# Kernel tuning notes

Measured on AMD Instinct MI355X. Metric: run time of the kernel, lower is better.

## Reference

```python
import jax, jax.numpy as jnp
import numpy as np

EPS = 1e-6

def elu1(x):
    return jax.nn.elu(x) + 1.0

def causal_linear_attention(q, k, v, chunk=128):
    # q,k,v: [b,h,s,d]; standard (elu+1) linear attention with causal cumulative
    # normalization, computed chunk-wise with a lax.scan carrying the kv state.
    b, h, s, d = q.shape
    sq, sk = elu1(q), elu1(k)
    nc = s // chunk
    rs = lambda x: x.reshape(b, h, nc, chunk, d).transpose(2, 0, 1, 3, 4)  # [nc,b,h,L,d]
    sqc, skc, vc = rs(sq), rs(sk), rs(v)
    mask = jnp.tril(jnp.ones((chunk, chunk), dtype=q.dtype))

    def step(carry, xs):
        S, z = carry  # S: [b,h,d,d] running sum of k^T v; z: [b,h,d] running sum of k
        qc, kc, vcc = xs
        scores = jnp.einsum('bhid,bhjd->bhij', qc, kc) * mask
        num = jnp.einsum('bhij,bhje->bhie', scores, vcc) + jnp.einsum('bhid,bhde->bhie', qc, S)
        den = scores.sum(-1) + jnp.einsum('bhid,bhd->bhi', qc, z)
        out = num / jnp.clip(den, EPS)[..., None]
        S = S + jnp.einsum('bhjd,bhje->bhde', kc, vcc)
        z = z + kc.sum(2)
        return (S, z), out

    S0 = jnp.zeros((b, h, d, d), q.dtype)
    z0 = jnp.zeros((b, h, d), q.dtype)
    _, outs = jax.lax.scan(step, (S0, z0), (sqc, skc, vc))
    return outs.transpose(1, 2, 0, 3, 4).reshape(b, h, s, d)

def setup_inputs() -> dict:
    B, S, H, NH, NM = 2, 4096, 2048, 16, 4
    HD = H // NH
    key = jax.random.key(0)
    ks = jax.random.split(key, 12)
    p = lambda k, shp: (jax.random.normal(k, shp, dtype=jnp.float32) * 0.02)
    return {
        'hidden_states': jax.random.normal(ks[0], (B, S, H), dtype=jnp.float32),
        'w_q': p(ks[1], (H, H)),
        'w_k': p(ks[2], (H, H)),
        'w_v': p(ks[3], (H, H)),
        'w_o': p(ks[4], (H, H)),
        'eg_w1': p(ks[5], (H // 4, H)),
        'eg_b1': jnp.zeros((H // 4,), jnp.float32),
        'eg_w2': p(ks[6], (1, H // 4)),
        'eg_b2': jnp.zeros((1,), jnp.float32),
        'memory_gate': jnp.zeros((NH,), jnp.float32),
        'fine_memories': jax.random.uniform(ks[7], (NM, NH, HD, HD), dtype=jnp.float32) * 0.1,
        'fine_memory_norms': jax.random.uniform(ks[8], (NM, NH, HD), dtype=jnp.float32) + 0.1,
    }

def reference(hidden_states, w_q, w_k, w_v, w_o, eg_w1, eg_b1, eg_w2, eg_b2,
              memory_gate, fine_memories, fine_memory_norms):
    B, S, H = hidden_states.shape
    NH = memory_gate.shape[0]
    HD = H // NH
    split = lambda x: x.reshape(B, S, NH, HD).transpose(0, 2, 1, 3)  # [b,h,s,d]
    q = split(hidden_states @ w_q.T)
    k = split(hidden_states @ w_k.T)
    v = split(hidden_states @ w_v.T)
    sq = elu1(q)

    # coarse memory = sum of fine banks
    M = fine_memories.sum(0)            # [h,d,d]
    z = fine_memory_norms.sum(0)        # [h,d]
    a_c = jnp.einsum('bhsd,hde->bhse', sq, M)
    n_c = jnp.clip(jnp.einsum('bhsd,hd->bhs', sq, z), EPS)[..., None]
    out_coarse = jnp.where(z.sum() < EPS, 0.0, a_c / n_c)

    # fine-grained retrieval over banks, softmax-weighted by relevance
    a_f = jnp.einsum('bhsd,mhde->mbhse', sq, fine_memories)
    n_f = jnp.einsum('bhsd,mhd->mbhs', sq, fine_memory_norms)
    bank_dead = (fine_memory_norms.sum((1, 2)) < EPS)[:, None, None, None, None]
    outs = jnp.where(bank_dead, 0.0, a_f / jnp.clip(n_f, EPS)[..., None])
    rel = n_f.mean(-1)  # [m,b,h]
    w = jax.nn.softmax(rel, axis=0)[..., None, None]  # [m,b,h,1,1]
    out_fine = (outs * w).sum(0)

    # learned expansion gate from coarse representation
    coarse_repr = out_coarse.transpose(0, 2, 1, 3).reshape(B, S, H)
    gprob = jax.nn.sigmoid(jax.nn.relu(coarse_repr @ eg_w1.T + eg_b1) @ eg_w2.T + eg_b2)  # [b,s,1]
    exp_prob = gprob.transpose(0, 2, 1)[..., None]  # [b,1,s,1]

    memory_output = exp_prob * out_fine + (1.0 - exp_prob) * out_coarse
    local_output = causal_linear_attention(q, k, v)
    gate = jax.nn.sigmoid(memory_gate).reshape(1, NH, 1, 1)
    output = gate * memory_output + (1.0 - gate) * local_output
    output = output.transpose(0, 2, 1, 3).reshape(B, S, H)
    return output @ w_o.T
```

## Files before the change

kernel.cpp:

```cpp
#include <hip/hip_runtime.h>

typedef unsigned short ush;
typedef short s16x8 __attribute__((ext_vector_type(8)));
typedef float f32x4 __attribute__((ext_vector_type(4)));

#define Bv 2
#define Sv 4096
#define Hv 2048
#define NHv 16
#define HDv 128
#define NMv 4
#define Tv (Bv*Sv)
#define CHv 128
#define NCv (Sv/CHv)
#define EPSf 1e-6f
#define NTHc ((size_t)Tv*Hv)

__device__ __forceinline__ float b2f(ush u){ return __uint_as_float(((unsigned)u)<<16); }
__device__ __forceinline__ ush f2b(float f){
  unsigned x = __float_as_uint(f);
  return (ush)((x + 0x7fffu + ((x>>16)&1u)) >> 16);
}
__device__ __forceinline__ float lo16(unsigned u){ return b2f((ush)(u & 0xffffu)); }
__device__ __forceinline__ float hi16(unsigned u){ return b2f((ush)(u >> 16)); }
__device__ __forceinline__ unsigned pack2(float a, float b){ return (unsigned)f2b(a) | ((unsigned)f2b(b) << 16); }
__device__ __forceinline__ float elu1f(float x){ return x > 0.f ? x + 1.f : __expf(x); }
__device__ __forceinline__ float sigm(float x){ return 1.f/(1.f + __expf(-x)); }

__device__ __forceinline__ void gload_lds16(const ush* g, ush* l) {
  __builtin_amdgcn_global_load_lds((const __attribute__((address_space(1))) unsigned int*)g,
                                   (__attribute__((address_space(3))) unsigned int*)l, 16, 0, 0);
}

__global__ void probe_kernel(float* out, float val){ out[0] = val; }

__global__ __launch_bounds__(256)
void cvt_kernel(const float* __restrict__ in, ush* __restrict__ out, int n8)
{
  int i = blockIdx.x * 256 + threadIdx.x;
  if (i >= n8) return;
  const float4* p = (const float4*)in + (size_t)i*2;
  float4 x = p[0], y = p[1];
  ushort4 a; a.x=f2b(x.x); a.y=f2b(x.y); a.z=f2b(x.z); a.w=f2b(x.w);
  ushort4 b; b.x=f2b(y.x); b.y=f2b(y.y); b.z=f2b(y.z); b.w=f2b(y.w);
  *(ushort4*)(out + (size_t)i*8)     = a;
  *(ushort4*)(out + (size_t)i*8 + 4) = b;
}

__global__ __launch_bounds__(256)
void fmt_kernel(const float* __restrict__ fm, ush* __restrict__ fmt)
{
  int mh = blockIdx.x;
  const float* src = fm + (size_t)mh*HDv*HDv;
  ush* dst = fmt + (size_t)mh*HDv*HDv;
  __shared__ ush T[HDv][HDv+4];
  #pragma unroll 4
  for (int l = 0; l < 64; ++l) {
    int idx = threadIdx.x + l*256;
    int d = idx >> 7, e = idx & 127;
    T[d][e] = f2b(src[idx]);
  }
  __syncthreads();
  #pragma unroll 4
  for (int l = 0; l < 64; ++l) {
    int idx = threadIdx.x + l*256;
    int e = idx >> 7, d = idx & 127;
    dst[idx] = T[d][e];
  }
}

__global__ __launch_bounds__(256)
void tp_kernel(const ush* __restrict__ src, ush* __restrict__ dst)
{
  int blk = blockIdx.x;
  int st = blk & 31, bh = blk >> 5;
  int h = bh & 15, b = bh >> 4;
  size_t t0 = (size_t)b*Sv + st*128;
  int hcol = h*HDv;
  __shared__ __align__(16) ush T[128*128];
  int tid = threadIdx.x;
  #pragma unroll
  for (int l = 0; l < 8; ++l) {
    int idx = tid + l*256;
    int row = idx >> 4, c8 = (idx & 15) << 3;
    *(uint4*)(T + row*128 + c8) = *(const uint4*)(src + (t0 + row)*Hv + hcol + c8);
  }
  __syncthreads();
  #pragma unroll
  for (int l = 0; l < 8; ++l) {
    int idx = tid + l*256;
    int d = idx & 127, t8 = (idx >> 7) << 3;
    ush tmp[8];
    #pragma unroll
    for (int q = 0; q < 8; ++q) tmp[q] = T[(t8 + q)*128 + d];
    *(uint4*)(dst + ((size_t)bh*HDv + d)*Sv + st*128 + t8) = *(uint4*)tmp;
  }
}

template<int OBF, int EPQ>
__global__ __launch_bounds__(512)
void gemm8(const ush* __restrict__ A, const ush* __restrict__ B,
           const float* __restrict__ bias,
           ush* __restrict__ C0, ush* __restrict__ C1, ush* __restrict__ C2,
           float* __restrict__ Cf, int N, int K)
{
  __shared__ __align__(16) ush LDS[3*16384 + 3*8192];
  ush* Atb = LDS;
  ush* Btb = LDS + 3*16384;
  const int tid = threadIdx.x, lane = tid & 63, w = tid >> 6;
  const int wr = w >> 1, wn = w & 1;
  const int la = lane & 15, lk = lane >> 4;

  int bid = blockIdx.x;
  int NBX = N >> 7;
  int by, bx;
  if ((NBX & 7) == 0) {
    int bpx = NBX >> 3;
    int xcd = bid & 7;
    int idx = bid >> 3;
    bx = xcd*bpx + idx % bpx;
    by = idx / bpx;
  } else {
    bx = bid % NBX;
    by = bid / NBX;
  }
  int bm = by << 8, bn = bx << 7;

  auto stage = [&](int t){
    int kt = t << 6;
    ush* Ad = Atb + (t % 3) * 16384;
    ush* Bd = Btb + (t % 3) * 8192;
    #pragma unroll
    for (int c = 0; c < 4; ++c) {
      int idx = tid + c*512;
      int row = idx >> 3, sl = idx & 7;
      gload_lds16(A + (size_t)(bm + row)*K + kt + ((sl ^ (row & 7))*8),
                  Ad + (w*64 + c*512)*8);
    }
    #pragma unroll
    for (int c = 0; c < 2; ++c) {
      int idx = tid + c*512;
      int row = idx >> 3, sl = idx & 7;
      gload_lds16(B + (size_t)(bn + row)*K + kt + ((sl ^ (row & 7))*8),
                  Bd + (w*64 + c*512)*8);
    }
  };

  f32x4 acc[4][4];
  #pragma unroll
  for (int i = 0; i < 4; ++i)
    #pragma unroll
    for (int j = 0; j < 4; ++j) acc[i][j] = (f32x4){0.f,0.f,0.f,0.f};

  stage(0);
  stage(1);
  const int nt = 32;
  for (int t = 0; t < nt; ++t) {
    if (t < nt-2) {
      stage(t + 2);
      asm volatile("s_waitcnt vmcnt(12)" ::: "memory");
    } else if (t == nt-2) {
      asm volatile("s_waitcnt vmcnt(6)" ::: "memory");
    } else {
      asm volatile("s_waitcnt vmcnt(0)" ::: "memory");
    }
    __builtin_amdgcn_s_barrier();
    __builtin_amdgcn_sched_barrier(0);

    const ush* Ab = Atb + (t % 3) * 16384;
    const ush* Bb = Btb + (t % 3) * 8192;
    __builtin_amdgcn_s_setprio(1);
    #pragma unroll
    for (int kk = 0; kk < 2; ++kk) {
      s16x8 a[4], b[4];
      int ks = kk*4 + lk;
      #pragma unroll
      for (int f = 0; f < 4; ++f) {
        int ar = wr*64 + f*16 + la;
        a[f] = *(const s16x8*)(Ab + ar*64 + ((ks ^ (ar & 7))*8));
        int br = wn*64 + f*16 + la;
        b[f] = *(const s16x8*)(Bb + br*64 + ((ks ^ (br & 7))*8));
      }
      #pragma unroll
      for (int i = 0; i < 4; ++i)
        #pragma unroll
        for (int j = 0; j < 4; ++j)
          acc[i][j] = __builtin_amdgcn_mfma_f32_16x16x32_bf16(a[i], b[j], acc[i][j], 0, 0, 0);
    }
    __builtin_amdgcn_s_setprio(0);
    __builtin_amdgcn_sched_barrier(0);
    __builtin_amdgcn_s_barrier();
  }

  int seg = bn >> 11;
  if (OBF) {
    ush* Cb = LDS;
    #pragma unroll
    for (int i = 0; i < 4; ++i)
      #pragma unroll
      for (int j = 0; j < 4; ++j)
        #pragma unroll
        for (int r = 0; r < 4; ++r) {
          int row = wr*64 + i*16 + lk*4 + r;
          int col = wn*64 + j*16 + la;
          float v = acc[i][j][r];
          if (EPQ == 1 && seg < 2) v = elu1f(v);
          Cb[row*136 + col] = f2b(v);
        }
    __syncthreads();
    ush* outp = (seg == 0) ? C0 : (seg == 1) ? C1 : C2;
    int col0 = bn & 2047;
    #pragma unroll
    for (int l = 0; l < 8; ++l) {
      int chunk = tid + l*512;
      int row = chunk >> 4, cc = chunk & 15;
      *(uint4*)(outp + (size_t)(bm + row)*2048 + col0 + cc*8) = *(const uint4*)(Cb + row*136 + cc*8);
    }
  } else {
    float* Cb = (float*)LDS;
    #pragma unroll
    for (int i = 0; i < 4; ++i)
      #pragma unroll
      for (int j = 0; j < 4; ++j)
        #pragma unroll
        for (int r = 0; r < 4; ++r) {
          int row = wr*64 + i*16 + lk*4 + r;
          int col = wn*64 + j*16 + la;
          float v = acc[i][j][r];
          if (EPQ == 2) v = fmaxf(v + bias[bn + col], 0.f);
          Cb[row*132 + col] = v;
        }
    __syncthreads();
    #pragma unroll
    for (int l = 0; l < 16; ++l) {
      int chunk = tid + l*512;
      int row = chunk >> 5, cc = chunk & 31;
      *(float4*)(Cf + (size_t)(bm + row)*N + bn + cc*4) = *(const float4*)(Cb + row*132 + cc*4);
    }
  }
}

__global__ void prep_kernel(const float* __restrict__ norms, const float* __restrict__ mg,
                            float* __restrict__ zsum, float* __restrict__ gate)
{
  int idx = blockIdx.x * 256 + threadIdx.x;
  if (idx < NHv*HDv) {
    float s = 0.f;
    #pragma unroll
    for (int m = 0; m < NMv; ++m) s += norms[m*NHv*HDv + idx];
    zsum[idx] = s;
  }
  if (idx < NHv) gate[idx] = sigm(mg[idx]);
}

__global__ void prep2_kernel(const float* __restrict__ norms, float* __restrict__ bdead,
                             float* __restrict__ ztot, float* __restrict__ rel)
{
  int tid = threadIdx.x;
  float pm[NMv] = {0.f,0.f,0.f,0.f};
  for (int i = tid; i < NHv*HDv; i += 256)
    #pragma unroll
    for (int m = 0; m < NMv; ++m) pm[m] += norms[m*NHv*HDv + i];
  __shared__ float red[4][NMv];
  #pragma unroll
  for (int m = 0; m < NMv; ++m) {
    float v = pm[m];
    for (int off = 32; off; off >>= 1) v += __shfl_down(v, off, 64);
    if ((tid & 63) == 0) red[tid >> 6][m] = v;
  }
  __syncthreads();
  if (tid == 0) {
    float tot = 0.f;
    #pragma unroll
    for (int m = 0; m < NMv; ++m) {
      float s = red[0][m] + red[1][m] + red[2][m] + red[3][m];
      bdead[m] = (s < EPSf) ? 1.f : 0.f;
      tot += s;
    }
    ztot[0] = tot;
  }
  if (tid < NMv*Bv*NHv) rel[tid] = 0.f;
}

__global__ __launch_bounds__(256)
void nf_kernel(const ush* __restrict__ sq, const float* __restrict__ norms,
               const float* __restrict__ zsum, float* __restrict__ nf5,
               float* __restrict__ rel)
{
  int blk = blockIdx.x;
  int st = blk % (Sv/256);
  int bh = blk / (Sv/256);
  int h = bh & 15, b = bh >> 4;
  int tid = threadIdx.x;
  __shared__ float nrm[5][HDv];
  for (int i = tid; i < 5*HDv; i += 256) {
    int m = i / HDv, d = i % HDv;
    nrm[m][d] = (m < NMv) ? norms[(m*NHv + h)*HDv + d] : zsum[h*HDv + d];
  }
  __syncthreads();
  int s = st*256 + tid;
  size_t t = (size_t)b*Sv + s;
  const ush* qp = sq + t*Hv + h*HDv;
  float acc[5] = {0.f,0.f,0.f,0.f,0.f};
  #pragma unroll 4
  for (int d0 = 0; d0 < HDv; d0 += 8) {
    uint4 u = *(const uint4*)(qp + d0);
    float q[8];
    q[0]=lo16(u.x); q[1]=hi16(u.x); q[2]=lo16(u.y); q[3]=hi16(u.y);
    q[4]=lo16(u.z); q[5]=hi16(u.z); q[6]=lo16(u.w); q[7]=hi16(u.w);
    #pragma unroll
    for (int e = 0; e < 8; ++e)
      #pragma unroll
      for (int m = 0; m < 5; ++m) acc[m] = fmaf(q[e], nrm[m][d0+e], acc[m]);
  }
  #pragma unroll
  for (int m = 0; m < 5; ++m) nf5[((size_t)m*Bv*NHv + bh)*Sv + s] = acc[m];
  __shared__ float redl[4][NMv];
  #pragma unroll
  for (int m = 0; m < NMv; ++m) {
    float v = acc[m];
    for (int off = 32; off; off >>= 1) v += __shfl_down(v, off, 64);
    if ((tid & 63) == 0) redl[tid >> 6][m] = v;
  }
  __syncthreads();
  if (tid < NMv) {
    float sm = redl[0][tid] + redl[1][tid] + redl[2][tid] + redl[3][tid];
    atomicAdd(&rel[tid*Bv*NHv + bh], sm);
  }
}

__global__ void softmax_rel(const float* __restrict__ rel, float* __restrict__ wsm)
{
  int i = threadIdx.x;
  if (i >= Bv*NHv) return;
  float r[NMv], mx = -1e30f;
  #pragma unroll
  for (int m = 0; m < NMv; ++m) { r[m] = rel[m*Bv*NHv + i] / (float)Sv; mx = fmaxf(mx, r[m]); }
  float se = 0.f;
  #pragma unroll
  for (int m = 0; m < NMv; ++m) { r[m] = __expf(r[m] - mx); se += r[m]; }
  #pragma unroll
  for (int m = 0; m < NMv; ++m) wsm[m*Bv*NHv + i] = r[m] / se;
}

__global__ __launch_bounds__(512)
void finecoarse_mfma(const ush* __restrict__ sq, const ush* __restrict__ fmt,
                     const float* __restrict__ nf5, const float* __restrict__ wsm,
                     const float* __restrict__ bdead, const float* __restrict__ ztot,
                     ush* __restrict__ fineO, ush* __restrict__ coarseO)
{
  __shared__ __align__(16) ush Qs[2*128*64];
  __shared__ __align__(16) ush Fs[2*128*64];
  __shared__ float scl[NMv][128];
  __shared__ float csc[128];

  int blk = blockIdx.x;
  int tt = blk & 31; int bh = blk >> 5;
  int h = bh & 15, b = bh >> 4;
  size_t t0 = (size_t)b*Sv + tt*128;
  int hcol = h*HDv;
  int tid = threadIdx.x;
  int lane = tid & 63, w = tid >> 6;
  int wr = w >> 2, wc = w & 3;
  int srow = lane >> 3, sslot = lane & 7;
  int la = lane & 15, lk = lane >> 4;

  #pragma unroll
  for (int kh = 0; kh < 2; ++kh)
    #pragma unroll
    for (int r = 0; r < 2; ++r) {
      int row = r*64 + w*8 + srow;
      int kg = sslot ^ (row & 7);
      gload_lds16(sq + (t0 + row)*Hv + hcol + kh*64 + kg*8,
                  Qs + kh*8192 + (r*64 + w*8)*64);
    }
  if (tid < 128) {
    int s = tt*128 + tid;
    float nc = nf5[((size_t)4*Bv*NHv + bh)*Sv + s];
    csc[tid] = (ztot[0] >= EPSf) ? 1.f/fmaxf(nc, EPSf) : 0.f;
    #pragma unroll
    for (int m = 0; m < NMv; ++m) {
      float nfm = nf5[((size_t)m*Bv*NHv + bh)*Sv + s];
      scl[m][tid] = (bdead[m] > 0.5f) ? 0.f : wsm[m*Bv*NHv + bh]/fmaxf(nfm, EPSf);
    }
  }

  f32x4 accF[4][2], accC[4][2];
  #pragma unroll
  for (int i = 0; i < 4; ++i)
    #pragma unroll
    for (int j = 0; j < 2; ++j) { accF[i][j] = (f32x4){0,0,0,0}; accC[i][j] = (f32x4){0,0,0,0}; }

  for (int m = 0; m < NMv; ++m) {
    const ush* F = fmt + (size_t)(m*NHv + h)*HDv*HDv;
    #pragma unroll
    for (int kh = 0; kh < 2; ++kh)
      #pragma unroll
      for (int r = 0; r < 2; ++r) {
        int row = r*64 + w*8 + srow;
        int kg = sslot ^ (row & 7);
        gload_lds16(F + (size_t)row*HDv + kh*64 + kg*8,
                    Fs + kh*8192 + (r*64 + w*8)*64);
      }
    __syncthreads();
    f32x4 P[4][2];
    #pragma unroll
    for (int i = 0; i < 4; ++i)
      #pragma unroll
      for (int j = 0; j < 2; ++j) P[i][j] = (f32x4){0,0,0,0};
    #pragma unroll
    for (int kh = 0; kh < 2; ++kh)
      #pragma unroll
      for (int ks = 0; ks < 2; ++ks) {
        s16x8 a[4], bq[2];
        int kslot = ks*4 + lk;
        #pragma unroll
        for (int f = 0; f < 4; ++f) {
          int arow = wr*64 + f*16 + la;
          a[f] = *(const s16x8*)(Qs + kh*8192 + arow*64 + ((kslot ^ (arow & 7))*8));
        }
        #pragma unroll
        for (int f = 0; f < 2; ++f) {
          int brow = wc*32 + f*16 + la;
          bq[f] = *(const s16x8*)(Fs + kh*8192 + brow*64 + ((kslot ^ (brow & 7))*8));
        }
        #pragma unroll
        for (int i = 0; i < 4; ++i)
          #pragma unroll
          for (int j = 0; j < 2; ++j)
            P[i][j] = __builtin_amdgcn_mfma_f32_16x16x32_bf16(a[i], bq[j], P[i][j], 0, 0, 0);
      }
    #pragma unroll
    for (int i = 0; i < 4; ++i) {
      float sm[4];
      #pragma unroll
      for (int r = 0; r < 4; ++r) sm[r] = scl[m][wr*64 + i*16 + lk*4 + r];
      #pragma unroll
      for (int j = 0; j < 2; ++j)
        #pragma unroll
        for (int r = 0; r < 4; ++r) {
          accF[i][j][r] = fmaf(sm[r], P[i][j][r], accF[i][j][r]);
          accC[i][j][r] += P[i][j][r];
        }
    }
    __syncthreads();
  }
  #pragma unroll
  for (int i = 0; i < 4; ++i)
    #pragma unroll
    for (int r = 0; r < 4; ++r) {
      int row = wr*64 + i*16 + lk*4 + r;
      float cs = csc[row];
      size_t gro = (t0 + row)*Hv + hcol;
      #pragma unroll
      for (int j = 0; j < 2; ++j) {
        int col = wc*32 + j*16 + la;
        fineO[gro + col]   = f2b(accF[i][j][r]);
        coarseO[gro + col] = f2b(accC[i][j][r]*cs);
      }
    }
}

__global__ __launch_bounds__(64)
void gprob_kernel(const float* __restrict__ g1, const float* __restrict__ w2,
                  const float* __restrict__ b2, float* __restrict__ gprob)
{
  int t = blockIdx.x, l = threadIdx.x;
  float s = 0.f;
  #pragma unroll
  for (int i = l; i < Hv/4; i += 64) s = fmaf(g1[(size_t)t*(Hv/4) + i], w2[i], s);
  for (int off = 32; off; off >>= 1) s += __shfl_down(s, off, 64);
  if (l == 0) gprob[t] = sigm(s + b2[0]);
}

__global__ __launch_bounds__(512)
void kv_chunk_mfma(const ush* __restrict__ kT, const ush* __restrict__ vT,
                   float* __restrict__ KVc, float* __restrict__ zc)
{
  __shared__ __align__(16) ush Vt[128*128];
  __shared__ __align__(16) ush Kt[128*128];
  int blk = blockIdx.x;
  int c = blk & 31, bh = blk >> 5;
  const ush* kg = kT + (size_t)bh*HDv*Sv + c*CHv;
  const ush* vg = vT + (size_t)bh*HDv*Sv + c*CHv;
  int tid = threadIdx.x, lane = tid & 63, w = tid >> 6;
  int wr = w >> 2, wc = w & 3;
  int la = lane & 15, lk = lane >> 4;
  int srow4 = lane >> 4, sslot = lane & 15;

  #pragma unroll
  for (int r = 0; r < 4; ++r) {
    int row = r*32 + w*4 + srow4;
    int slot = sslot ^ (row & 7);
    gload_lds16(vg + (size_t)row*Sv + slot*8, Vt + (r*32 + w*4)*128);
    gload_lds16(kg + (size_t)row*Sv + slot*8, Kt + (r*32 + w*4)*128);
  }
  __syncthreads();

  if (tid < 128) {
    float zacc = 0.f;
    int rx = tid & 7;
    #pragma unroll
    for (int s = 0; s < 16; ++s) {
      const ush* p = Kt + tid*128 + ((s ^ rx)*8);
      #pragma unroll
      for (int q = 0; q < 8; ++q) zacc += b2f(p[q]);
    }
    zc[(size_t)blk*HDv + tid] = zacc;
  }

  f32x4 acc[4][2];
  #pragma unroll
  for (int i = 0; i < 4; ++i)
    #pragma unroll
    for (int j = 0; j < 2; ++j) acc[i][j] = (f32x4){0,0,0,0};
  #pragma unroll
  for (int kw = 0; kw < 4; ++kw) {
    s16x8 a[4], b[2];
    int slot = kw*4 + lk;
    #pragma unroll
    for (int f = 0; f < 4; ++f) {
      int ar = wr*64 + f*16 + la;
      a[f] = *(const s16x8*)(Vt + ar*128 + ((slot ^ (ar & 7))*8));
    }
    #pragma unroll
    for (int f = 0; f < 2; ++f) {
      int br = wc*32 + f*16 + la;
      b[f] = *(const s16x8*)(Kt + br*128 + ((slot ^ (br & 7))*8));
    }
    #pragma unroll
    for (int i = 0; i < 4; ++i)
      #pragma unroll
      for (int j = 0; j < 2; ++j)
        acc[i][j] = __builtin_amdgcn_mfma_f32_16x16x32_bf16(a[i], b[j], acc[i][j], 0, 0, 0);
  }
  size_t obase = (size_t)blk*(HDv*HDv);
  #pragma unroll
  for (int i = 0; i < 4; ++i)
    #pragma unroll
    for (int j = 0; j < 2; ++j)
      #pragma unroll
      for (int r = 0; r < 4; ++r) {
        int e = wr*64 + i*16 + lk*4 + r;
        int d = wc*32 + j*16 + la;
        KVc[obase + e*HDv + d] = acc[i][j][r];
      }
}

__global__ __launch_bounds__(256)
void scan_kernel(const float* __restrict__ KVc, ush* __restrict__ kvt, float* __restrict__ zc)
{
  int blk = blockIdx.x;
  int dg = blk & 7; int bh = blk >> 3;
  int tid = threadIdx.x;
  float Sreg[8];
  #pragma unroll
  for (int k = 0; k < 8; ++k) Sreg[k] = 0.f;
  float zreg = 0.f;
  for (int c = 0; c < NCv; ++c) {
    size_t base = ((size_t)bh*NCv + c)*(HDv*HDv) + dg*2048;
    #pragma unroll
    for (int k = 0; k < 8; ++k) {
      size_t idx = base + tid + k*256;
      float tmp = KVc[idx];
      kvt[idx] = f2b(Sreg[k]);
      Sreg[k] += tmp;
    }
    if (dg == 0 && tid < HDv) {
      size_t zb = ((size_t)bh*NCv + c)*HDv + tid;
      float tmp = zc[zb];
      zc[zb] = zreg;
      zreg += tmp;
    }
  }
}

__global__ __launch_bounds__(512)
void attn_chunk_mfma(const ush* __restrict__ sq, const ush* __restrict__ sk,
                     const ush* __restrict__ vT, const ush* __restrict__ kvt,
                     const float* __restrict__ zc, ush* __restrict__ outl)
{
  __shared__ __align__(16) ush Qs[128*128];
  __shared__ __align__(16) ush Ks[128*128];
  __shared__ __align__(16) ush Vs[128*128];
  __shared__ __align__(16) ush Ss[128*128];
  __shared__ float densP[4][128];
  __shared__ float dens[128];

  int blk = blockIdx.x;
  int c = blk & 31, bh = blk >> 5;
  int h = bh & 15, b = bh >> 4;
  size_t t0 = (size_t)b*Sv + c*CHv;
  int hcol = h*HDv;
  int tid = threadIdx.x, lane = tid & 63, w = tid >> 6;
  int wr = w >> 2, wc = w & 3;
  int la = lane & 15, lk = lane >> 4;
  int srow4 = lane >> 4, sslot = lane & 15;
  const float* zcg = zc + (size_t)blk*HDv;

  const ush* qg = sq + t0*Hv + hcol;
  const ush* kg = sk + t0*Hv + hcol;
  const ush* vg = vT + (size_t)bh*HDv*Sv + c*CHv;
  const ush* sg = kvt + (size_t)blk*(HDv*HDv);
  #pragma unroll
  for (int r = 0; r < 4; ++r) {
    int row = r*32 + w*4 + srow4;
    int slot = sslot ^ (row & 7);
    int lb = (r*32 + w*4)*128;
    gload_lds16(qg + (size_t)row*Hv + slot*8, Qs + lb);
    gload_lds16(kg + (size_t)row*Hv + slot*8, Ks + lb);
    gload_lds16(vg + (size_t)row*Sv + slot*8, Vs + lb);
    gload_lds16(sg + row*HDv + slot*8, Ss + lb);
  }
  __syncthreads();

  f32x4 sc[4][2];
  #pragma unroll
  for (int i = 0; i < 4; ++i)
    #pragma unroll
    for (int j = 0; j < 2; ++j) sc[i][j] = (f32x4){0,0,0,0};
  #pragma unroll
  for (int kw = 0; kw < 4; ++kw) {
    s16x8 a[4], b[2];
    int slot = kw*4 + lk;
    #pragma unroll
    for (int f = 0; f < 4; ++f) {
      int ar = wr*64 + f*16 + la;
      a[f] = *(const s16x8*)(Qs + ar*128 + ((slot ^ (ar & 7))*8));
    }
    #pragma unroll
    for (int f = 0; f < 2; ++f) {
      int br = wc*32 + f*16 + la;
      b[f] = *(const s16x8*)(Ks + br*128 + ((slot ^ (br & 7))*8));
    }
    #pragma unroll
    for (int i = 0; i < 4; ++i)
      #pragma unroll
      for (int j = 0; j < 2; ++j)
        sc[i][j] = __builtin_amdgcn_mfma_f32_16x16x32_bf16(a[i], b[j], sc[i][j], 0, 0, 0);
  }
  __syncthreads();
  #pragma unroll
  for (int i = 0; i < 4; ++i)
    #pragma unroll
    for (int j = 0; j < 2; ++j)
      #pragma unroll
      for (int r = 0; r < 4; ++r) {
        int ii = wr*64 + i*16 + lk*4 + r;
        int jj = wc*32 + j*16 + la;
        float v = (jj <= ii) ? sc[i][j][r] : 0.f;
        Ks[ii*128 + (((jj >> 3) ^ (ii & 7))*8) + (jj & 7)] = f2b(v);
      }
  __syncthreads();

  {
    int row = tid & 127, qt = tid >> 7;
    int rx = row & 7;
    float s = 0.f;
    #pragma unroll
    for (int s8 = 0; s8 < 4; ++s8) {
      int slot = qt*4 + s8;
      const ush* p  = Ks + row*128 + ((slot ^ rx)*8);
      const ush* pq = Qs + row*128 + ((slot ^ rx)*8);
      #pragma unroll
      for (int q = 0; q < 8; ++q) s += b2f(p[q]);
      #pragma unroll
      for (int q = 0; q < 8; ++q) s = fmaf(b2f(pq[q]), zcg[slot*8 + q], s);
    }
    densP[qt][row] = s;
  }
  __syncthreads();
  if (tid < 128)
    dens[tid] = fmaxf(densP[0][tid] + densP[1][tid] + densP[2][tid] + densP[3][tid], EPSf);
  __syncthreads();

  f32x4 acc[4][2];
  #pragma unroll
  for (int i = 0; i < 4; ++i)
    #pragma unroll
    for (int j = 0; j < 2; ++j) acc[i][j] = (f32x4){0,0,0,0};
  #pragma unroll
  for (int kw = 0; kw < 4; ++kw) {
    s16x8 a[4], b[2];
    int slot = kw*4 + lk;
    #pragma unroll
    for (int f = 0; f < 4; ++f) {
      int ar = wr*64 + f*16 + la;
      a[f] = *(const s16x8*)(Ks + ar*128 + ((slot ^ (ar & 7))*8));
    }
    #pragma unroll
    for (int f = 0; f < 2; ++f) {
      int br = wc*32 + f*16 + la;
      b[f] = *(const s16x8*)(Vs + br*128 + ((slot ^ (br & 7))*8));
    }
    #pragma unroll
    for (int i = 0; i < 4; ++i)
      #pragma unroll
      for (int j = 0; j < 2; ++j)
        acc[i][j] = __builtin_amdgcn_mfma_f32_16x16x32_bf16(a[i], b[j], acc[i][j], 0, 0, 0);
  }
  #pragma unroll
  for (int kw = 0; kw < 4; ++kw) {
    s16x8 a[4], b[2];
    int slot = kw*4 + lk;
    #pragma unroll
    for (int f = 0; f < 4; ++f) {
      int ar = wr*64 + f*16 + la;
      a[f] = *(const s16x8*)(Qs + ar*128 + ((slot ^ (ar & 7))*8));
    }
    #pragma unroll
    for (int f = 0; f < 2; ++f) {
      int br = wc*32 + f*16 + la;
      b[f] = *(const s16x8*)(Ss + br*128 + ((slot ^ (br & 7))*8));
    }
    #pragma unroll
    for (int i = 0; i < 4; ++i)
      #pragma unroll
      for (int j = 0; j < 2; ++j)
        acc[i][j] = __builtin_amdgcn_mfma_f32_16x16x32_bf16(a[i], b[j], acc[i][j], 0, 0, 0);
  }
  #pragma unroll
  for (int i = 0; i < 4; ++i)
    #pragma unroll
    for (int r = 0; r < 4; ++r) {
      int ii = wr*64 + i*16 + lk*4 + r;
      float inv = 1.f / dens[ii];
      ush* orow = outl + (t0 + ii)*Hv + hcol;
      #pragma unroll
      for (int j = 0; j < 2; ++j) {
        int ee = wc*32 + j*16 + la;
        orow[ee] = f2b(acc[i][j][r]*inv);
      }
    }
}

__global__ __launch_bounds__(256)
void combine_kernel(const ush* __restrict__ fine, const ush* __restrict__ coarse,
                    const ush* __restrict__ local, const float* __restrict__ gprob,
                    const float* __restrict__ gate, ush* __restrict__ comb)
{
  size_t idx = (size_t)blockIdx.x * 256 + threadIdx.x;
  if (idx >= NTHc/8) return;
  size_t fi = idx * 8;
  int t = (int)(fi / Hv);
  int h = (int)((fi % Hv) >> 7);
  float g = gate[h];
  float p = gprob[t];
  uint4 uf = *(const uint4*)(fine + fi);
  uint4 uc = *(const uint4*)(coarse + fi);
  uint4 ul = *(const uint4*)(local + fi);
  uint4 o;
  unsigned* ufp = (unsigned*)&uf; unsigned* ucp = (unsigned*)&uc;
  unsigned* ulp = (unsigned*)&ul; unsigned* op = (unsigned*)&o;
  #pragma unroll
  for (int wq = 0; wq < 4; ++wq) {
    float f0 = lo16(ufp[wq]), f1 = hi16(ufp[wq]);
    float c0 = lo16(ucp[wq]), c1 = hi16(ucp[wq]);
    float l0 = lo16(ulp[wq]), l1 = hi16(ulp[wq]);
    float o0 = g*(p*f0 + (1.f-p)*c0) + (1.f-g)*l0;
    float o1 = g*(p*f1 + (1.f-p)*c1) + (1.f-g)*l1;
    op[wq] = pack2(o0, o1);
  }
  *(uint4*)(comb + fi) = o;
}

extern "C" void kernel_launch(void* const* d_in, const int* in_sizes, int n_in,
                              void* d_out, int out_size, void* d_ws, size_t ws_size,
                              hipStream_t stream)
{
  (void)in_sizes; (void)n_in; (void)out_size;
  const float* hs    = (const float*)d_in[0];
  const float* w_q   = (const float*)d_in[1];
  const float* w_k   = (const float*)d_in[2];
  const float* w_v   = (const float*)d_in[3];
  const float* w_o   = (const float*)d_in[4];
  const float* eg_w1 = (const float*)d_in[5];
  const float* eg_b1 = (const float*)d_in[6];
  const float* eg_w2 = (const float*)d_in[7];
  const float* eg_b2 = (const float*)d_in[8];
  const float* mg    = (const float*)d_in[9];
  const float* fm    = (const float*)d_in[10];
  const float* norms = (const float*)d_in[11];

  probe_kernel<<<1, 1, 0, stream>>>((float*)d_out, (float)(ws_size >> 20));

  char* W = (char*)d_ws;
  size_t o = 0;
  auto take = [&](size_t bytes) -> char* {
    char* p = W + o;
    o += (bytes + 255) & ~(size_t)255;
    return p;
  };
  ush* hs_bf = (ush*)take(NTHc * 2);
  ush* kT = hs_bf;
  ush* local_bf = hs_bf;
  char* R2 = take(NTHc * 4);
  ush* wq_bf = (ush*)R2;
  ush* wk_bf = (ush*)(R2 + (size_t)Hv*Hv*2);
  ush* wv_bf = (ush*)(R2 + (size_t)Hv*Hv*4);
  float* kvc = (float*)R2;
  ush* fine_bf = (ush*)R2;
  float* g1 = (float*)(R2 + NTHc*2);
  ush* wo_bf   = (ush*)take((size_t)Hv*Hv*2);
  ush* egw1_bf = (ush*)take((size_t)(Hv/4)*Hv*2);
  ush* sq_bf = (ush*)take(NTHc * 2);  ush* comb = sq_bf;
  ush* sk_bf = (ush*)take(NTHc * 2);
  ush* v_bf  = (ush*)take(NTHc * 2);
  ush* kvt_bf = v_bf;
  ush* vT = (ush*)take(NTHc * 2);
  ush* coarse_bf = vT;
  float* zcb  = (float*)take((size_t)Bv*NHv*NCv*HDv * 4);
  float* nf5  = (float*)take((size_t)5*Bv*NHv*Sv * 4);
  ush* fmt_bf = (ush*)take((size_t)NMv*NHv*HDv*HDv * 2);
  float* rel  = (float*)take(NMv*Bv*NHv * 4);
  float* wsm  = (float*)take(NMv*Bv*NHv * 4);
  float* gprob= (float*)take((size_t)Tv * 4);
  float* zsum = (float*)take(NHv*HDv * 4);
  float* gate = (float*)take(NHv * 4);
  float* bdead= (float*)take(NMv * 4);
  float* ztot = (float*)take(4);
  if (ws_size < o) return;

  cvt_kernel<<<(int)(NTHc/8/256), 256, 0, stream>>>(hs, hs_bf, (int)(NTHc/8));
  cvt_kernel<<<(int)((size_t)Hv*Hv/8/256), 256, 0, stream>>>(w_q, wq_bf, Hv*Hv/8);
  cvt_kernel<<<(int)((size_t)Hv*Hv/8/256), 256, 0, stream>>>(w_k, wk_bf, Hv*Hv/8);
  cvt_kernel<<<(int)((size_t)Hv*Hv/8/256), 256, 0, stream>>>(w_v, wv_bf, Hv*Hv/8);
  cvt_kernel<<<(int)((size_t)Hv*Hv/8/256), 256, 0, stream>>>(w_o, wo_bf, Hv*Hv/8);
  cvt_kernel<<<(int)((size_t)(Hv/4)*Hv/8/256), 256, 0, stream>>>(eg_w1, egw1_bf, (Hv/4)*Hv/8);
  fmt_kernel<<<NMv*NHv, 256, 0, stream>>>(fm, fmt_bf);

  prep_kernel<<<(NHv*HDv + 255)/256, 256, 0, stream>>>(norms, mg, zsum, gate);
  prep2_kernel<<<1, 256, 0, stream>>>(norms, bdead, ztot, rel);

  gemm8<1,1><<<(6144/128)*(Tv/256), 512, 0, stream>>>(hs_bf, wq_bf, nullptr,
                                                      sq_bf, sk_bf, v_bf, nullptr, 6144, Hv);

  tp_kernel<<<Bv*NHv*32, 256, 0, stream>>>(sk_bf, kT);
  tp_kernel<<<Bv*NHv*32, 256, 0, stream>>>(v_bf, vT);

  nf_kernel<<<Bv*NHv*(Sv/256), 256, 0, stream>>>(sq_bf, norms, zsum, nf5, rel);
  softmax_rel<<<1, 64, 0, stream>>>(rel, wsm);

  kv_chunk_mfma<<<Bv*NHv*NCv, 512, 0, stream>>>(kT, vT, kvc, zcb);
  scan_kernel<<<Bv*NHv*8, 256, 0, stream>>>(kvc, kvt_bf, zcb);
  attn_chunk_mfma<<<Bv*NHv*NCv, 512, 0, stream>>>(sq_bf, sk_bf, vT, kvt_bf, zcb, local_bf);

  finecoarse_mfma<<<Bv*NHv*32, 512, 0, stream>>>(sq_bf, fmt_bf, nf5, wsm, bdead, ztot, fine_bf, coarse_bf);

  gemm8<0,2><<<(512/128)*(Tv/256), 512, 0, stream>>>(coarse_bf, egw1_bf, eg_b1,
                                                     nullptr, nullptr, nullptr, g1, 512, Hv);
  gprob_kernel<<<Tv, 64, 0, stream>>>(g1, eg_w2, eg_b2, gprob);

  combine_kernel<<<(int)(NTHc/8/256), 256, 0, stream>>>(fine_bf, coarse_bf, local_bf, gprob, gate, comb);

  gemm8<0,0><<<(2048/128)*(Tv/256), 512, 0, stream>>>(comb, wo_bf, nullptr,
                                                      nullptr, nullptr, nullptr, (float*)d_out, 2048, Hv);
}
```

Baseline: 618.1 us.

## Add 256x256-tile GEMM kernel for QKV and output projections

Introduces gemm9, a GEMM with 256x256 output tiles, 8 waves in a 2x4 layout and double-buffered K=64 LDS staging. The next tile's global loads are interleaved between MFMA groups, with setprio hints and an XCD-aware block remap. It replaces the 128-wide gemm8 for the fused QKV projection and the output projection to raise arithmetic intensity per loaded byte. The larger tile uses 128KB of LDS and many accumulator registers, which limits occupancy and leaves fewer blocks to fill the GPU.

```diff
diff --git a/kernel.cpp b/kernel.cpp
--- a/kernel.cpp
+++ b/kernel.cpp
@@ -94,6 +94,194 @@
     #pragma unroll
     for (int q = 0; q < 8; ++q) tmp[q] = T[(t8 + q)*128 + d];
     *(uint4*)(dst + ((size_t)bh*HDv + d)*Sv + st*128 + t8) = *(uint4*)tmp;
+  }
+}
+
+template<int OBF, int EPQ>
+__global__ __launch_bounds__(512)
+void gemm9(const ush* __restrict__ A, const ush* __restrict__ B,
+           ush* __restrict__ C0, ush* __restrict__ C1, ush* __restrict__ C2,
+           float* __restrict__ Cf, int N, int K)
+{
+  __shared__ __align__(16) ush LDSm[65536];
+  const int tid = threadIdx.x, lane = tid & 63, w = tid >> 6;
+  const int wr = w >> 2, wn = w & 3;
+  const int la = lane & 15, lk = lane >> 4;
+
+  int bid = blockIdx.x;
+  int NBX = N >> 8;
+  int by, bx;
+  if ((NBX & 7) == 0) {
+    int bpx = NBX >> 3;
+    int xcd = bid & 7;
+    int idx = bid >> 3;
+    bx = xcd*bpx + idx % bpx;
+    by = idx / bpx;
+  } else {
+    bx = bid % NBX;
+    by = bid / NBX;
+  }
+  int bm = by << 8, bn = bx << 8;
+
+  auto stageA = [&](int t, int c){
+    ush* Ad = LDSm + (t & 1)*32768 + c*8192;
+    int kt = t << 6;
+    #pragma unroll
+    for (int l = 0; l < 2; ++l) {
+      int u = tid + l*512;
+      int row = u >> 3, sl = u & 7;
+      gload_lds16(A + (size_t)(bm + c*128 + row)*K + kt + ((sl ^ (row & 7))*8),
+                  Ad + (l*512 + w*64)*8);
+    }
+  };
+  auto stageB = [&](int t, int c){
+    ush* Bd = LDSm + (t & 1)*32768 + 16384 + c*8192;
+    int kt = t << 6;
+    #pragma unroll
+    for (int l = 0; l < 2; ++l) {
+      int u = tid + l*512;
+      int row = u >> 3, sl = u & 7;
+      gload_lds16(B + (size_t)(bn + c*128 + row)*K + kt + ((sl ^ (row & 7))*8),
+                  Bd + (l*512 + w*64)*8);
+    }
+  };
+
+  f32x4 acc[8][4];
+  #pragma unroll
+  for (int i = 0; i < 8; ++i)
+    #pragma unroll
+    for (int j = 0; j < 4; ++j) acc[i][j] = (f32x4){0.f,0.f,0.f,0.f};
+
+  stageA(0,0); stageA(0,1); stageB(0,0); stageB(0,1);
+  asm volatile("s_waitcnt vmcnt(0)" ::: "memory");
+  __builtin_amdgcn_s_barrier();
+  __builtin_amdgcn_sched_barrier(0);
+
+  const int nt = K >> 6;
+  for (int t = 0; t < nt; ++t) {
+    const ush* Ab = LDSm + (t & 1)*32768;
+    const ush* Bb = Ab + 16384;
+    if (t + 1 < nt) { stageA(t+1, 0); stageA(t+1, 1); }
+    s16x8 b0[4], a0[4];
+    __builtin_amdgcn_s_setprio(1);
+    #pragma unroll
+    for (int g = 0; g < 4; ++g) {
+      int br = wn*64 + g*16 + la;
+      b0[g] = *(const s16x8*)(Bb + br*64 + ((lk ^ (br & 7))*8));
+    }
+    #pragma unroll
+    for (int f = 0; f < 4; ++f) {
+      int ar = wr*128 + f*16 + la;
+      a0[f] = *(const s16x8*)(Ab + ar*64 + ((lk ^ (ar & 7))*8));
+    }
+    #pragma unroll
+    for (int f = 0; f < 4; ++f)
+      #pragma unroll
+      for (int g = 0; g < 4; ++g)
+        acc[f][g] = __builtin_amdgcn_mfma_f32_16x16x32_bf16(a0[f], b0[g], acc[f][g], 0, 0, 0);
+    __builtin_amdgcn_s_setprio(0);
+    if (t + 1 < nt) { stageB(t+1, 0); stageB(t+1, 1); }
+    __builtin_amdgcn_s_setprio(1);
+    #pragma unroll
+    for (int f = 0; f < 4; ++f) {
+      int ar = wr*128 + (f+4)*16 + la;
+      a0[f] = *(const s16x8*)(Ab + ar*64 + ((lk ^ (ar & 7))*8));
+    }
+    #pragma unroll
+    for (int f = 0; f < 4; ++f)
+      #pragma unroll
+      for (int g = 0; g < 4; ++g)
+        acc[f+4][g] = __builtin_amdgcn_mfma_f32_16x16x32_bf16(a0[f], b0[g], acc[f+4][g], 0, 0, 0);
+    int ks1 = 4 + lk;
+    #pragma unroll
+    for (int g = 0; g < 4; ++g) {
+      int br = wn*64 + g*16 + la;
+      b0[g] = *(const s16x8*)(Bb + br*64 + ((ks1 ^ (br & 7))*8));
+    }
+    #pragma unroll
+    for (int f = 0; f < 4; ++f) {
+      int ar = wr*128 + f*16 + la;
+      a0[f] = *(const s16x8*)(Ab + ar*64 + ((ks1 ^ (ar & 7))*8));
+    }
+    #pragma unroll
+    for (int f = 0; f < 4; ++f)
+      #pragma unroll
+      for (int g = 0; g < 4; ++g)
+        acc[f][g] = __builtin_amdgcn_mfma_f32_16x16x32_bf16(a0[f], b0[g], acc[f][g], 0, 0, 0);
+    #pragma unroll
+    for (int f = 0; f < 4; ++f) {
+      int ar = wr*128 + (f+4)*16 + la;
+      a0[f] = *(const s16x8*)(Ab + ar*64 + ((ks1 ^ (ar & 7))*8));
+    }
+    #pragma unroll
+    for (int f = 0; f < 4; ++f)
+      #pragma unroll
+      for (int g = 0; g < 4; ++g)
+        acc[f+4][g] = __builtin_amdgcn_mfma_f32_16x16x32_bf16(a0[f], b0[g], acc[f+4][g], 0, 0, 0);
+    __builtin_amdgcn_s_setprio(0);
+    __builtin_amdgcn_sched_barrier(0);
+    asm volatile("s_waitcnt vmcnt(0)" ::: "memory");
+    __builtin_amdgcn_s_barrier();
+    __builtin_amdgcn_sched_barrier(0);
+  }
+
+  int seg = bn >> 11;
+  if (OBF) {
+    ush* Cb = LDSm;
+    ush* outp = (seg == 0) ? C0 : (seg == 1) ? C1 : C2;
+    int col0 = bn & 2047;
+    #pragma unroll
+    for (int h = 0; h < 2; ++h) {
+      if (h) __syncthreads();
+      if (wr == h) {
+        #pragma unroll
+        for (int f = 0; f < 8; ++f)
+          #pragma unroll
+          for (int g = 0; g < 4; ++g)
+            #pragma unroll
+            for (int r = 0; r < 4; ++r) {
+              int row = f*16 + lk*4 + r;
+              int col = wn*64 + g*16 + la;
+              float v = acc[f][g][r];
+              if (EPQ == 1 && seg < 2) v = elu1f(v);
+              Cb[row*264 + col] = f2b(v);
+            }
+      }
+      __syncthreads();
+      #pragma unroll
+      for (int l = 0; l < 8; ++l) {
+        int chunk = tid + l*512;
+        int row = chunk >> 5, cc = chunk & 31;
+        *(uint4*)(outp + (size_t)(bm + h*128 + row)*2048 + col0 + cc*8) = *(const uint4*)(Cb + row*264 + cc*8);
+      }
+    }
+  } else {
+    float* Cb = (float*)LDSm;
+    #pragma unroll
+    for (int h2 = 0; h2 < 4; ++h2) {
+      if (h2) __syncthreads();
+      if (wr == (h2 >> 1)) {
+        #pragma unroll
+        for (int f = 0; f < 4; ++f) {
+          int fa = (h2 & 1)*4 + f;
+          #pragma unroll
+          for (int g = 0; g < 4; ++g)
+            #pragma unroll
+            for (int r = 0; r < 4; ++r) {
+              int row = f*16 + lk*4 + r;
+              int col = wn*64 + g*16 + la;
+              Cb[row*260 + col] = acc[fa][g][r];
+            }
+        }
+      }
+      __syncthreads();
+      #pragma unroll
+      for (int l = 0; l < 8; ++l) {
+        int chunk = tid + l*512;
+        int row = chunk >> 6, cc = chunk & 63;
+        *(float4*)(Cf + (size_t)(bm + h2*64 + row)*N + bn + cc*4) = *(const float4*)(Cb + row*260 + cc*4);
+      }
+    }
   }
 }
 
@@ -832,7 +1020,7 @@
   prep_kernel<<<(NHv*HDv + 255)/256, 256, 0, stream>>>(norms, mg, zsum, gate);
   prep2_kernel<<<1, 256, 0, stream>>>(norms, bdead, ztot, rel);
 
-  gemm8<1,1><<<(6144/128)*(Tv/256), 512, 0, stream>>>(hs_bf, wq_bf, nullptr,
+  gemm9<1,1><<<(6144/256)*(Tv/256), 512, 0, stream>>>(hs_bf, wq_bf,
                                                       sq_bf, sk_bf, v_bf, nullptr, 6144, Hv);
 
   tp_kernel<<<Bv*NHv*32, 256, 0, stream>>>(sk_bf, kT);
@@ -853,6 +1041,6 @@
 
   combine_kernel<<<(int)(NTHc/8/256), 256, 0, stream>>>(fine_bf, coarse_bf, local_bf, gprob, gate, comb);
 
-  gemm8<0,0><<<(2048/128)*(Tv/256), 512, 0, stream>>>(comb, wo_bf, nullptr,
+  gemm9<0,0><<<(2048/256)*(Tv/256), 512, 0, stream>>>(comb, wo_bf,
                                                       nullptr, nullptr, nullptr, (float*)d_out, 2048, Hv);
 }
```

Measured after the change: 557.7 us. -9.8%, faster.
